# Performance work log

Hardware: AMD Instinct MI355X
Metric: run time of the kernel (lower is better)

Reference implementation:

```python
import jax, jax.numpy as jnp
import numpy as np

B = 131072
F = 512

def setup_inputs() -> dict:
    key = jax.random.key(0)
    kx, kq = jax.random.split(key)
    x = jax.random.normal(kx, (B, F), dtype=jnp.float32)
    # Q param: xavier-normal init, then strictly-lower-triangular entries zeroed
    # (mask = tril(ones, diagonal=-1); Q.masked_fill_(mask, 0)).
    std = float(np.sqrt(2.0 / (F + F)))
    Q = jax.random.normal(kq, (F, F), dtype=jnp.float32) * std
    Q = jnp.triu(Q)  # zero strictly-lower triangle, keep diagonal
    return {"x": x, "Q": Q}

def reference(x, Q):
    # Original: diag(x @ Q @ x.T).view(-1, 1).
    # Equivalent per-row bilinear form, avoiding the [B, B] intermediate:
    # out[b] = sum_f sum_g x[b,f] Q[f,g] x[b,g]
    xQ = x @ Q                           # [B, F]
    out = jnp.sum(xQ * x, axis=1, keepdims=True)  # [B, 1]
    return out
```

## Files before the change

kernel.cpp:

```cpp
#include <hip/hip_runtime.h>
#include <hip/hip_bf16.h>

typedef __bf16 bf16_t;
typedef __bf16 bf16x8 __attribute__((ext_vector_type(8)));
typedef __bf16 bf16x4 __attribute__((ext_vector_type(4)));
typedef float f32x4 __attribute__((ext_vector_type(4)));

#define FDIM 512
#define NTHR 512
#define BROWS 128
#define NBLK 1024

__global__ void qtrans_kernel(const float* __restrict__ Q, bf16_t* __restrict__ Qt) {
    __shared__ float t[32][33];
    int tx = threadIdx.x & 31;
    int ty = threadIdx.x >> 5;
    int f0 = blockIdx.x * 32;
    int g0 = blockIdx.y * 32;
#pragma unroll
    for (int i = 0; i < 4; ++i)
        t[ty + 8 * i][tx] = Q[(size_t)(f0 + ty + 8 * i) * FDIM + g0 + tx];
    __syncthreads();
#pragma unroll
    for (int i = 0; i < 4; ++i)
        Qt[(size_t)(g0 + ty + 8 * i) * FDIM + f0 + tx] = (bf16_t)t[tx][ty + 8 * i];
}

__global__ __launch_bounds__(NTHR, 4) void bilinear_kernel(
    const float* __restrict__ x, const bf16_t* __restrict__ Qt,
    float* __restrict__ out)
{
    __shared__ bf16_t panel[2][32 * FDIM];

    const int tid = threadIdx.x;
    const int w   = tid >> 6;
    const int l   = tid & 63;
    const int col = l & 15;
    const int kg  = l >> 4;

    const int row0w = blockIdx.x * BROWS + w * 16;

    const float* arow = x + (size_t)(row0w + col) * FDIM + kg * 8;
    bf16x8 a[16];
#pragma unroll
    for (int ks = 0; ks < 16; ++ks) {
        float4 f0 = *(const float4*)(arow + ks * 32);
        float4 f1 = *(const float4*)(arow + ks * 32 + 4);
        bf16x8 v;
        v[0] = (bf16_t)f0.x; v[1] = (bf16_t)f0.y; v[2] = (bf16_t)f0.z; v[3] = (bf16_t)f0.w;
        v[4] = (bf16_t)f1.x; v[5] = (bf16_t)f1.y; v[6] = (bf16_t)f1.z; v[7] = (bf16_t)f1.w;
        a[ks] = v;
        if ((ks & 3) == 3) __builtin_amdgcn_sched_barrier(0);
    }

    {
        const int c = w;
#pragma unroll
        for (int i = 0; i < 4; ++i) {
            int cc = i * 8 + w;
            if (l < 4) {
                bf16x8 q = *(const bf16x8*)(Qt + (size_t)cc * FDIM + l * 8);
                int e = cc * FDIM + ((l * 8) ^ ((cc & 15) << 3));
                *(bf16x8*)(&panel[0][0] + e) = q;
            }
        }
        (void)c;
    }
    __syncthreads();

    float rs[4] = {0.f, 0.f, 0.f, 0.f};

#pragma unroll 1
    for (int p = 0; p < 16; ++p) {
        const int buf = p & 1;
        const bf16_t* pb = &panel[buf][0];

        if (p + 1 < 16) {
            const int pn = p + 1;
            const int lim = 4 * (pn + 1);
            bf16_t* pw = &panel[buf ^ 1][0];
#pragma unroll
            for (int i = 0; i < 4; ++i) {
                int cc = i * 8 + w;
                if (l < lim) {
                    bf16x8 q = *(const bf16x8*)(Qt + (size_t)(pn * 32 + cc) * FDIM + l * 8);
                    int e = cc * FDIM + ((l * 8) ^ ((cc & 15) << 3));
                    *(bf16x8*)(pw + e) = q;
                }
            }
        }

        f32x4 acc0, acc1;
#pragma unroll
        for (int j = 0; j < 4; ++j) { acc0[j] = 0.f; acc1[j] = 0.f; }

        const int kswz = col << 3;
#pragma unroll
        for (int ks = 0; ks < 16; ++ks) {
            if (ks <= p) {
                int kk = (ks * 32 + kg * 8) ^ kswz;
                bf16x8 b0 = *(const bf16x8*)(pb + col * FDIM + kk);
                bf16x8 b1 = *(const bf16x8*)(pb + (16 + col) * FDIM + kk);
                acc0 = __builtin_amdgcn_mfma_f32_16x16x32_bf16(a[ks], b0, acc0, 0, 0, 0);
                acc1 = __builtin_amdgcn_mfma_f32_16x16x32_bf16(a[ks], b1, acc1, 0, 0, 0);
            }
        }

        const float* xe = x + (size_t)(row0w + kg * 4) * FDIM + p * 32 + col;
#pragma unroll
        for (int j = 0; j < 4; ++j) {
            float e0 = xe[(size_t)j * FDIM];
            float e1 = xe[(size_t)j * FDIM + 16];
            rs[j] += acc0[j] * e0 + acc1[j] * e1;
        }

        __syncthreads();
    }

#pragma unroll
    for (int j = 0; j < 4; ++j) {
        float v2 = rs[j];
        v2 += __shfl_xor(v2, 1);
        v2 += __shfl_xor(v2, 2);
        v2 += __shfl_xor(v2, 4);
        v2 += __shfl_xor(v2, 8);
        rs[j] = v2;
    }
    if (col == 0) {
#pragma unroll
        for (int j = 0; j < 4; ++j)
            out[row0w + kg * 4 + j] = rs[j];
    }
}

extern "C" void kernel_launch(void* const* d_in, const int* in_sizes, int n_in,
                              void* d_out, int out_size, void* d_ws, size_t ws_size,
                              hipStream_t stream) {
    const float* x = (const float*)d_in[0];
    const float* Q = (const float*)d_in[1];
    float* out = (float*)d_out;
    bf16_t* Qt = (bf16_t*)d_ws;

    dim3 tgrid(FDIM / 32, FDIM / 32);
    qtrans_kernel<<<tgrid, 256, 0, stream>>>(Q, Qt);
    bilinear_kernel<<<NBLK, NTHR, 0, stream>>>(x, Qt, out);
}
```

Measured before the change: 122.0 us.

## Split K dimension across wave pairs, halving rows per block

Each block now covers 64 rows instead of 128, and pairs of waves share a 16-row tile, each handling alternating K-slices (even/odd). This halves the A-fragment registers per wave and doubles the grid, aiming to raise occupancy and shorten each wave's serial MFMA chain. Partial row sums are combined through shared memory with an extra barrier. In exchange, each Q panel load from global/LDS serves half as many rows, so Q traffic per row doubles.

```diff
diff --git a/kernel.cpp b/kernel.cpp
--- a/kernel.cpp
+++ b/kernel.cpp
@@ -3,13 +3,12 @@
 
 typedef __bf16 bf16_t;
 typedef __bf16 bf16x8 __attribute__((ext_vector_type(8)));
-typedef __bf16 bf16x4 __attribute__((ext_vector_type(4)));
 typedef float f32x4 __attribute__((ext_vector_type(4)));
 
 #define FDIM 512
 #define NTHR 512
-#define BROWS 128
-#define NBLK 1024
+#define BROWS 64
+#define NBLK 2048
 
 __global__ void qtrans_kernel(const float* __restrict__ Q, bf16_t* __restrict__ Qt) {
     __shared__ float t[32][33];
@@ -31,40 +30,40 @@
     float* __restrict__ out)
 {
     __shared__ bf16_t panel[2][32 * FDIM];
+    __shared__ float rsum[8][16];
 
     const int tid = threadIdx.x;
-    const int w   = tid >> 6;
-    const int l   = tid & 63;
-    const int col = l & 15;
-    const int kg  = l >> 4;
+    const int w    = tid >> 6;
+    const int l    = tid & 63;
+    const int col  = l & 15;
+    const int kg   = l >> 4;
+    const int mt   = w >> 1;
+    const int kpar = w & 1;
 
-    const int row0w = blockIdx.x * BROWS + w * 16;
+    const int row0w = blockIdx.x * BROWS + mt * 16;
 
     const float* arow = x + (size_t)(row0w + col) * FDIM + kg * 8;
-    bf16x8 a[16];
+    bf16x8 a[8];
 #pragma unroll
-    for (int ks = 0; ks < 16; ++ks) {
+    for (int i = 0; i < 8; ++i) {
+        const int ks = 2 * i + kpar;
         float4 f0 = *(const float4*)(arow + ks * 32);
         float4 f1 = *(const float4*)(arow + ks * 32 + 4);
         bf16x8 v;
         v[0] = (bf16_t)f0.x; v[1] = (bf16_t)f0.y; v[2] = (bf16_t)f0.z; v[3] = (bf16_t)f0.w;
         v[4] = (bf16_t)f1.x; v[5] = (bf16_t)f1.y; v[6] = (bf16_t)f1.z; v[7] = (bf16_t)f1.w;
-        a[ks] = v;
-        if ((ks & 3) == 3) __builtin_amdgcn_sched_barrier(0);
+        a[i] = v;
+        if ((i & 1) == 1) __builtin_amdgcn_sched_barrier(0);
     }
 
-    {
-        const int c = w;
 #pragma unroll
-        for (int i = 0; i < 4; ++i) {
-            int cc = i * 8 + w;
-            if (l < 4) {
-                bf16x8 q = *(const bf16x8*)(Qt + (size_t)cc * FDIM + l * 8);
-                int e = cc * FDIM + ((l * 8) ^ ((cc & 15) << 3));
-                *(bf16x8*)(&panel[0][0] + e) = q;
-            }
+    for (int i = 0; i < 4; ++i) {
+        int cc = i * 8 + w;
+        if (l < 4) {
+            bf16x8 q = *(const bf16x8*)(Qt + (size_t)cc * FDIM + l * 8);
+            int e = cc * FDIM + ((l * 8) ^ ((cc & 15) << 3));
+            *(bf16x8*)(&panel[0][0] + e) = q;
         }
-        (void)c;
     }
     __syncthreads();
 
@@ -96,22 +95,22 @@
 
         const int kswz = col << 3;
 #pragma unroll
-        for (int ks = 0; ks < 16; ++ks) {
+        for (int i = 0; i < 8; ++i) {
+            const int ks = 2 * i + kpar;
             if (ks <= p) {
                 int kk = (ks * 32 + kg * 8) ^ kswz;
                 bf16x8 b0 = *(const bf16x8*)(pb + col * FDIM + kk);
                 bf16x8 b1 = *(const bf16x8*)(pb + (16 + col) * FDIM + kk);
-                acc0 = __builtin_amdgcn_mfma_f32_16x16x32_bf16(a[ks], b0, acc0, 0, 0, 0);
-                acc1 = __builtin_amdgcn_mfma_f32_16x16x32_bf16(a[ks], b1, acc1, 0, 0, 0);
+                acc0 = __builtin_amdgcn_mfma_f32_16x16x32_bf16(a[i], b0, acc0, 0, 0, 0);
+                acc1 = __builtin_amdgcn_mfma_f32_16x16x32_bf16(a[i], b1, acc1, 0, 0, 0);
             }
         }
 
         const float* xe = x + (size_t)(row0w + kg * 4) * FDIM + p * 32 + col;
 #pragma unroll
         for (int j = 0; j < 4; ++j) {
-            float e0 = xe[(size_t)j * FDIM];
-            float e1 = xe[(size_t)j * FDIM + 16];
-            rs[j] += acc0[j] * e0 + acc1[j] * e1;
+            rs[j] += acc0[j] * xe[(size_t)j * FDIM]
+                   + acc1[j] * xe[(size_t)j * FDIM + 16];
         }
 
         __syncthreads();
@@ -129,7 +128,15 @@
     if (col == 0) {
 #pragma unroll
         for (int j = 0; j < 4; ++j)
-            out[row0w + kg * 4 + j] = rs[j];
+            rsum[w][kg * 4 + j] = rs[j];
+    }
+    __syncthreads();
+
+    if (tid < BROWS) {
+        int mtile = tid >> 4;
+        int i = tid & 15;
+        out[(size_t)blockIdx.x * BROWS + mtile * 16 + i] =
+            rsum[2 * mtile][i] + rsum[2 * mtile + 1][i];
     }
 }
 
```

Result: slower. 125.1 us (+2.5%).
